# Kernel optimization log

Measured on AMD Instinct MI355X. Metric: run time of the kernel, lower is better.

Reference implementation:

```python
import jax, jax.numpy as jnp
import numpy as np

OS = 14            # output_size
GRID = 2           # ceil(roi_size/OS) = ceil(28/14) = 2 (boxes are built 28x28, sampling_ratio=-1)
NODES = OS * OS    # 196 graph nodes
EPS = 1e-5         # BatchNorm eps
K, B, C, H, W = 256, 4, 256, 112, 112


def _bn_relu(x, g, b, m, v):
    # eval-mode BatchNorm2d followed by ReLU (bn_act_conv prefix)
    s = jax.lax.rsqrt(v + EPS)
    xn = (x - m[None, :, None, None]) * s[None, :, None, None]
    return jax.nn.relu(xn * g[None, :, None, None] + b[None, :, None, None])


def _conv(x, w, b, pad):
    y = jax.lax.conv_general_dilated(x, w, (1, 1), [(pad, pad), (pad, pad)],
                                     dimension_numbers=('NCHW', 'OIHW', 'NCHW'))
    return y + b[None, :, None, None]


def _roi_align(sem, boxes):
    # torchvision roi_align, spatial_scale=1.0, aligned=False, sampling_ratio=-1 (static grid=2)
    Bs, Cc, Hh, Ww = sem.shape
    bidx = boxes[:, 0].astype(jnp.int32)
    x1, y1, x2, y2 = boxes[:, 1], boxes[:, 2], boxes[:, 3], boxes[:, 4]
    bw = jnp.maximum(x2 - x1, 1.0) / OS
    bh = jnp.maximum(y2 - y1, 1.0) / OS
    t = (jnp.arange(OS * GRID, dtype=sem.dtype) + 0.5) / GRID   # pw*GRID+ix collapsed
    xs = x1[:, None] + bw[:, None] * t                          # [K, 28]
    ys = y1[:, None] + bh[:, None] * t

    def prep(c, L):
        m = (c >= -1.0) & (c <= L)
        cc = jnp.clip(c, 0.0, L - 1)
        lo = jnp.floor(cc).astype(jnp.int32)
        hi = jnp.minimum(lo + 1, L - 1)
        return m, lo, hi, cc - lo

    my, yl, yh, ly = prep(ys, Hh)
    mx, xl, xh, lx = prep(xs, Ww)
    semt = jnp.transpose(sem, (0, 2, 3, 1))  # [B,H,W,C]

    def gat(ya, xa):
        return semt[bidx[:, None, None], ya[:, :, None], xa[:, None, :]]  # [K,28,28,C]

    ly_ = ly[:, :, None, None]
    lx_ = lx[:, None, :, None]
    val = (gat(yl, xl) * (1 - ly_) * (1 - lx_) + gat(yl, xh) * (1 - ly_) * lx_
           + gat(yh, xl) * ly_ * (1 - lx_) + gat(yh, xh) * ly_ * lx_)
    val = jnp.where((my[:, :, None] & mx[:, None, :])[..., None], val, 0.0)
    val = val.reshape(-1, OS, GRID, OS, GRID, Cc).mean(axis=(2, 4))  # avg over sampling grid
    return jnp.transpose(val, (0, 3, 1, 2))  # [K,C,14,14]


def _gcn_agg(A, x):
    # PyG gcn_norm on a fully-connected weighted graph (self loops already present):
    # deg[j] = sum_i A[i,j] (scatter on col); out[j] = sum_i d^-1/2[i] A[i,j] d^-1/2[j] x[i]
    deg = A.sum(axis=1)                 # [K,196]
    dis = jax.lax.rsqrt(deg)            # sigmoid weights > 0 => no zero degree
    Nrm = dis[:, :, None] * A * dis[:, None, :]
    return jnp.einsum('kij,kif->kjf', Nrm, x)


def _forward(roi_feature, semantic, boxes,
             bn_sem_g, bn_sem_b, bn_sem_m, bn_sem_v, conv_sem_w, conv_sem_b,
             bn_fpn_g, bn_fpn_b, bn_fpn_m, bn_fpn_v, conv_fpn_w, conv_fpn_b,
             bn_aff_g, bn_aff_b, bn_aff_m, bn_aff_v, conv_aff_w, conv_aff_b,
             gcn1_w, gcn1_b, gcn2_w, gcn2_b):
    roi_sem = _roi_align(semantic, boxes)                                   # [K,256,14,14]
    a = (_conv(_bn_relu(roi_sem, bn_sem_g, bn_sem_b, bn_sem_m, bn_sem_v), conv_sem_w, conv_sem_b, 1)
         + _conv(_bn_relu(roi_feature, bn_fpn_g, bn_fpn_b, bn_fpn_m, bn_fpn_v), conv_fpn_w, conv_fpn_b, 1))
    aff = _conv(_bn_relu(a, bn_aff_g, bn_aff_b, bn_aff_m, bn_aff_v), conv_aff_w, conv_aff_b, 0)
    A = jax.nn.sigmoid(aff.reshape(-1, NODES, NODES))                       # [K,196,196]
    X = roi_feature.reshape(-1, C, NODES).transpose(0, 2, 1)                # [K,196,256] node feats
    x1 = jax.nn.relu(_gcn_agg(A, X @ gcn1_w) + gcn1_b)                      # GCNConv(256,16)+ReLU
    x2 = _gcn_agg(A, x1 @ gcn2_w) + gcn2_b                                  # GCNConv(16,256)
    emb = x2.transpose(0, 2, 1).reshape(-1, C, OS, OS)
    return roi_sem + emb


def setup_inputs() -> dict:
    key = jax.random.key(0)
    ks = jax.random.split(key, 24)
    roi_feature = jax.random.normal(ks[0], (K, C, OS, OS), jnp.float32)
    semantic = jax.random.normal(ks[1], (B, C, H, W), jnp.float32)
    bidx = jax.random.randint(ks[2], (K,), 0, B).astype(jnp.float32)
    xy = jax.random.uniform(ks[3], (K, 2), jnp.float32, 0.0, float(H - 28))
    boxes = jnp.concatenate([bidx[:, None], xy, xy + 28.0], axis=1)  # (idx,x1,y1,x2,y2), 28x28 boxes

    def bn(kg, c):
        k1, k2, k3, k4 = jax.random.split(kg, 4)
        return (jax.random.normal(k1, (c,)) * 0.1 + 1.0,
                jax.random.normal(k2, (c,)) * 0.1,
                jax.random.normal(k3, (c,)) * 0.1,
                jax.random.uniform(k4, (c,), jnp.float32, 0.5, 1.5))
    bn_sem = bn(ks[4], C); bn_fpn = bn(ks[5], C); bn_aff = bn(ks[6], 64)
    inp = {
        'roi_feature': roi_feature, 'semantic': semantic, 'boxes': boxes,
        'bn_sem_g': bn_sem[0], 'bn_sem_b': bn_sem[1], 'bn_sem_m': bn_sem[2], 'bn_sem_v': bn_sem[3],
        'conv_sem_w': jax.random.normal(ks[7], (64, C, 3, 3)) * 0.02,
        'conv_sem_b': jax.random.normal(ks[8], (64,)) * 0.02,
        'bn_fpn_g': bn_fpn[0], 'bn_fpn_b': bn_fpn[1], 'bn_fpn_m': bn_fpn[2], 'bn_fpn_v': bn_fpn[3],
        'conv_fpn_w': jax.random.normal(ks[9], (64, C, 3, 3)) * 0.02,
        'conv_fpn_b': jax.random.normal(ks[10], (64,)) * 0.02,
        'bn_aff_g': bn_aff[0], 'bn_aff_b': bn_aff[1], 'bn_aff_m': bn_aff[2], 'bn_aff_v': bn_aff[3],
        'conv_aff_w': jax.random.normal(ks[11], (NODES, 64, 1, 1)) * 0.05,
        'conv_aff_b': jax.random.normal(ks[12], (NODES,)) * 0.05,
        'gcn1_w': jax.random.normal(ks[13], (C, 16)) * 0.05,
        'gcn1_b': jax.random.normal(ks[14], (16,)) * 0.05,
        'gcn2_w': jax.random.normal(ks[15], (16, C)) * 0.05,
        'gcn2_b': jax.random.normal(ks[16], (C,)) * 0.05,
    }
    return inp


def reference(roi_feature, semantic, boxes,
              bn_sem_g, bn_sem_b, bn_sem_m, bn_sem_v, conv_sem_w, conv_sem_b,
              bn_fpn_g, bn_fpn_b, bn_fpn_m, bn_fpn_v, conv_fpn_w, conv_fpn_b,
              bn_aff_g, bn_aff_b, bn_aff_m, bn_aff_v, conv_aff_w, conv_aff_b,
              gcn1_w, gcn1_b, gcn2_w, gcn2_b):
    return _forward(roi_feature, semantic, boxes,
                    bn_sem_g, bn_sem_b, bn_sem_m, bn_sem_v, conv_sem_w, conv_sem_b,
                    bn_fpn_g, bn_fpn_b, bn_fpn_m, bn_fpn_v, conv_fpn_w, conv_fpn_b,
                    bn_aff_g, bn_aff_b, bn_aff_m, bn_aff_v, conv_aff_w, conv_aff_b,
                    gcn1_w, gcn1_b, gcn2_w, gcn2_b)
```

## Files before the change

### kernel.cpp

```cpp
#include <hip/hip_runtime.h>
#include <hip/hip_bf16.h>

#define KBOX 256
#define CCH  256
#define NODES 196
#define OS 14

typedef __attribute__((ext_vector_type(8))) short  bf16x8;
typedef __attribute__((ext_vector_type(8))) unsigned short u16x8;
typedef __attribute__((ext_vector_type(4))) float  f32x4;
typedef __attribute__((ext_vector_type(4))) short  s16x4;
typedef __attribute__((ext_vector_type(4))) int    i32x4;

__device__ __forceinline__ short f2bf(float x) {
  __hip_bfloat16 h = __float2bfloat16(x);
  return *reinterpret_cast<short*>(&h);
}
__device__ __forceinline__ float bf2f(unsigned short u) {
  unsigned int x = ((unsigned int)u) << 16;
  union { unsigned int i; float f; } c; c.i = x;
  return c.f;
}

#define MFMA16 __builtin_amdgcn_mfma_f32_16x16x32_bf16

__global__ __launch_bounds__(256) void prep_kernel(
    const float* __restrict__ bn_sem_g, const float* __restrict__ bn_sem_b,
    const float* __restrict__ bn_sem_m, const float* __restrict__ bn_sem_v,
    const float* __restrict__ conv_sem_w, const float* __restrict__ conv_sem_b,
    const float* __restrict__ bn_fpn_g, const float* __restrict__ bn_fpn_b,
    const float* __restrict__ bn_fpn_m, const float* __restrict__ bn_fpn_v,
    const float* __restrict__ conv_fpn_w, const float* __restrict__ conv_fpn_b,
    const float* __restrict__ bn_aff_g, const float* __restrict__ bn_aff_b,
    const float* __restrict__ bn_aff_m, const float* __restrict__ bn_aff_v,
    const float* __restrict__ conv_aff_w, const float* __restrict__ g1w,
    const float* __restrict__ g2w,
    float* __restrict__ ss_sem, float* __restrict__ ss_fpn, float* __restrict__ ss_aff2,
    short* __restrict__ wfrag, short* __restrict__ wafrag, short* __restrict__ g1wf,
    short* __restrict__ g2wf)
{
  int gid = blockIdx.x * blockDim.x + threadIdx.x;
  int gsz = gridDim.x * blockDim.x;
  for (int c = gid; c < 256; c += gsz) {
    float s = bn_sem_g[c] * rsqrtf(bn_sem_v[c] + 1e-5f);
    ss_sem[c] = s; ss_sem[256 + c] = bn_sem_b[c] - bn_sem_m[c] * s;
    float s2 = bn_fpn_g[c] * rsqrtf(bn_fpn_v[c] + 1e-5f);
    ss_fpn[c] = s2; ss_fpn[256 + c] = bn_fpn_b[c] - bn_fpn_m[c] * s2;
  }
  for (int c = gid; c < 64; c += gsz) {
    float s = bn_aff_g[c] * rsqrtf(bn_aff_v[c] + 1e-5f);
    float sh = bn_aff_b[c] - bn_aff_m[c] * s;
    float bias = conv_sem_b[c] + conv_fpn_b[c];
    ss_aff2[c] = s; ss_aff2[64 + c] = bias * s + sh;
  }
  for (int idx = gid; idx < 144 * 4 * 64 * 8; idx += gsz) {
    int e = idx & 7, lane = (idx >> 3) & 63, nt = (idx >> 9) & 3, kstep = idx >> 11;
    int src = kstep / 72, rem = kstep % 72, icc = rem / 9, pos = rem % 9;
    int ky = pos / 3, kx = pos % 3;
    int oc = nt * 16 + (lane & 15);
    int ic = icc * 32 + (lane >> 4) * 8 + e;
    const float* w = src ? conv_fpn_w : conv_sem_w;
    wfrag[idx] = f2bf(w[((oc * 256 + ic) * 3 + ky) * 3 + kx]);
  }
  for (int idx = gid; idx < 2 * 13 * 64 * 8; idx += gsz) {
    int t = idx;
    int e = t & 7; t >>= 3;
    int lane = t & 63; t >>= 6;
    int nt = t % 13; int s = t / 13;
    int i = nt * 16 + (lane & 15);
    int ic = s * 32 + (lane >> 4) * 8 + e;
    wafrag[idx] = f2bf(i < NODES ? conv_aff_w[i * 64 + ic] : 0.f);
  }
  for (int idx = gid; idx < 8 * 64 * 8; idx += gsz) {
    int e = idx & 7, lane = (idx >> 3) & 63, ks = idx >> 9;
    int ic = ks * 32 + (lane >> 4) * 8 + e;
    int f = lane & 15;
    g1wf[idx] = f2bf(g1w[ic * 16 + f]);
  }
  for (int idx = gid; idx < 16 * 64 * 8; idx += gsz) {
    int e = idx & 7, lane = (idx >> 3) & 63, ct = idx >> 9;
    int kk = (lane >> 4) * 8 + e;
    int c = ct * 16 + (lane & 15);
    g2wf[idx] = f2bf(kk < 16 ? g2w[kk * 256 + c] : 0.f);
  }
}

__global__ __launch_bounds__(256) void transpose_bf16_kernel(
    const float* __restrict__ in, unsigned short* __restrict__ out, int C, int HW)
{
  __shared__ float tile[64][65];
  int nh = (HW + 63) >> 6;
  int bi = blockIdx.x;
  int cb = bi % (C >> 6); bi /= (C >> 6);
  int hb = bi % nh; int b = bi / nh;
  int tx = threadIdx.x & 63, ty = threadIdx.x >> 6;
  const float* inb = in + (size_t)b * C * HW;
  unsigned short* outb = out + (size_t)b * HW * C;
  #pragma unroll
  for (int i = ty; i < 64; i += 4) {
    int c = cb * 64 + i, hw = hb * 64 + tx;
    tile[i][tx] = (hw < HW) ? inb[(size_t)c * HW + hw] : 0.f;
  }
  __syncthreads();
  int cp = threadIdx.x & 31;
  #pragma unroll
  for (int i = (int)(threadIdx.x >> 5); i < 64; i += 8) {
    int hw = hb * 64 + i;
    if (hw < HW) {
      ushort2 v;
      v.x = (unsigned short)f2bf(tile[cp * 2][i]);
      v.y = (unsigned short)f2bf(tile[cp * 2 + 1][i]);
      *(ushort2*)&outb[(size_t)hw * C + cb * 64 + cp * 2] = v;
    }
  }
}

__global__ __launch_bounds__(512) void roi_align_kernel(
    const unsigned short* __restrict__ semt, const float* __restrict__ boxes,
    unsigned short* __restrict__ roi_sem)
{
  __shared__ unsigned short slab[5][29][256];
  int kb = blockIdx.x / 7, g = blockIdx.x % 7;
  int tid = threadIdx.x, wave = tid >> 6, lane = tid & 63;
  const float* bx = boxes + kb * 5;
  int bb = (int)bx[0];
  float x1 = bx[1], y1 = bx[2];
  float xb = x1 + 0.5f, yv = y1 + 0.5f;
  int X0 = (int)floorf(xb); float fx = xb - (float)X0;
  int Y0 = (int)floorf(yv); float fy = yv - (float)Y0;
  const unsigned short* base = semt + (size_t)bb * 12544 * 256;
  #pragma unroll
  for (int i = 0; i < 19; ++i) {
    int s = wave + i * 8;
    if (s < 145) {
      int r = s / 29, xi = s - r * 29;
      int yr = min(Y0 + 4 * g + r, 111);
      int xc = min(X0 + xi, 111);
      *(s16x4*)&slab[r][xi][lane * 4] =
          *(const s16x4*)(base + ((size_t)yr * 112 + xc) * 256 + lane * 4);
    }
  }
  __syncthreads();
  int c2 = tid & 127, grp = tid >> 7;
  int oyl = grp >> 1, og = grp & 1;
  int rb = oyl * 2;
  float w0 = 1.f - fy;
  unsigned short* op = roi_sem + (((size_t)kb * NODES) + (2 * g + oyl) * OS) * 256 + c2 * 2;
  #pragma unroll
  for (int oxs = 0; oxs < 7; ++oxs) {
    int ox = og * 7 + oxs;
    float o0 = 0.f, o1 = 0.f;
    #pragma unroll
    for (int xi = 0; xi < 3; ++xi) {
      float xw = (xi == 0) ? (1.f - fx) : (xi == 1 ? 1.f : fx);
      const unsigned short* p0 = &slab[rb][2 * ox + xi][c2 * 2];
      const unsigned short* p1 = &slab[rb + 1][2 * ox + xi][c2 * 2];
      const unsigned short* p2 = &slab[rb + 2][2 * ox + xi][c2 * 2];
      o0 += xw * (w0 * bf2f(p0[0]) + bf2f(p1[0]) + fy * bf2f(p2[0]));
      o1 += xw * (w0 * bf2f(p0[1]) + bf2f(p1[1]) + fy * bf2f(p2[1]));
    }
    ushort2 v;
    v.x = (unsigned short)f2bf(o0 * 0.25f);
    v.y = (unsigned short)f2bf(o1 * 0.25f);
    *(ushort2*)(op + (size_t)ox * 256) = v;
  }
}

__global__ __launch_bounds__(512) void conv_ab_kernel(
    const unsigned short* __restrict__ roi_sem, const unsigned short* __restrict__ roif,
    const float* __restrict__ ss_sem, const float* __restrict__ ss_fpn,
    const float* __restrict__ ss_aff2, const short* __restrict__ wfrag,
    short* __restrict__ a_rel)
{
  __shared__ short inLDS[198 * 268];
  __shared__ float scA[64], cmbA[64];
  const int k = blockIdx.x;
  const int tid = threadIdx.x;
  const int wave = tid >> 6, lane = tid & 63;
  const int l15 = lane & 15, lq = lane >> 4;
  const int pg = wave >> 1, ng = wave & 1;
  const int p0 = (pg == 0) ? 0 : (pg * 2 + 1);
  const int p1 = p0 + ((pg == 0) ? 3 : 2);

  if (tid < 64) { scA[tid] = ss_aff2[tid]; cmbA[tid] = ss_aff2[64 + tid]; }
  if (tid < 34) {
    bf16x8 z = {};
    *(bf16x8*)&inLDS[196 * 268 + tid * 8] = z;
  }

  int oyA[13], oxA[13];
  #pragma unroll
  for (int mt = 0; mt < 13; ++mt) {
    int j = mt * 16 + l15;
    int oy = j / 14;
    oyA[mt] = oy; oxA[mt] = j - oy * 14;
  }
  const int c0 = (tid & 31) * 8;

  f32x4 acc[13][2];
  #pragma unroll
  for (int mt = 0; mt < 13; ++mt) {
    acc[mt][0] = f32x4{0.f, 0.f, 0.f, 0.f};
    acc[mt][1] = f32x4{0.f, 0.f, 0.f, 0.f};
  }

  for (int src = 0; src < 2; ++src) {
    const unsigned short* inp = (src ? roif : roi_sem) + (size_t)k * NODES * CCH;
    const float* ss = src ? ss_fpn : ss_sem;
    f32x4 sc0 = *(const f32x4*)(ss + c0);
    f32x4 sc1 = *(const f32x4*)(ss + c0 + 4);
    f32x4 sh0 = *(const f32x4*)(ss + 256 + c0);
    f32x4 sh1 = *(const f32x4*)(ss + 256 + c0 + 4);
    __syncthreads();
    #pragma unroll
    for (int i = 0; i < 12; ++i) {
      int j = (tid >> 5) + i * 16;
      u16x8 v = *(const u16x8*)(inp + (size_t)j * 256 + c0);
      bf16x8 pk;
      #pragma unroll
      for (int u = 0; u < 4; ++u) pk[u] = f2bf(fmaxf(bf2f(v[u]) * sc0[u] + sh0[u], 0.f));
      #pragma unroll
      for (int u = 0; u < 4; ++u) pk[4 + u] = f2bf(fmaxf(bf2f(v[4 + u]) * sc1[u] + sh1[u], 0.f));
      *(bf16x8*)&inLDS[j * 268 + c0] = pk;
    }
    if (tid < 128) {
      int j = 192 + (tid >> 5);
      u16x8 v = *(const u16x8*)(inp + (size_t)j * 256 + c0);
      bf16x8 pk;
      #pragma unroll
      for (int u = 0; u < 4; ++u) pk[u] = f2bf(fmaxf(bf2f(v[u]) * sc0[u] + sh0[u], 0.f));
      #pragma unroll
      for (int u = 0; u < 4; ++u) pk[4 + u] = f2bf(fmaxf(bf2f(v[4 + u]) * sc1[u] + sh1[u], 0.f));
      *(bf16x8*)&inLDS[j * 268 + c0] = pk;
    }
    __syncthreads();

    for (int pos = p0; pos < p1; ++pos) {
      int ky = pos / 3 - 1, kx = pos % 3 - 1;
      int np[13];
      #pragma unroll
      for (int mt = 0; mt < 13; ++mt) {
        int ny = oyA[mt] + ky, nx = oxA[mt] + kx;
        bool v = ((unsigned)ny < 14u) & ((unsigned)nx < 14u) & ((mt * 16 + l15) < 196);
        np[mt] = v ? (ny * 14 + nx) : 196;
      }
      #pragma unroll
      for (int icc = 0; icc < 8; ++icc) {
        const short* wp = wfrag +
            ((size_t)((src * 72 + icc * 9 + pos) * 4 + ng * 2) * 64 + lane) * 8;
        bf16x8 b0 = *(const bf16x8*)wp;
        bf16x8 b1 = *(const bf16x8*)(wp + 512);
        #pragma unroll
        for (int mt = 0; mt < 13; ++mt) {
          bf16x8 a = *(const bf16x8*)&inLDS[np[mt] * 268 + icc * 32 + lq * 8];
          acc[mt][0] = MFMA16(a, b0, acc[mt][0], 0, 0, 0);
          acc[mt][1] = MFMA16(a, b1, acc[mt][1], 0, 0, 0);
        }
      }
    }
  }

  float* red = (float*)inLDS;
  __syncthreads();
  if (pg == 1 || pg == 3) {
    float* dst = red + (size_t)((pg >> 1) * 2 + ng) * 6272;
    #pragma unroll
    for (int mt = 0; mt < 13; ++mt)
      #pragma unroll
      for (int nn = 0; nn < 2; ++nn)
        #pragma unroll
        for (int r = 0; r < 4; ++r) {
          int j = mt * 16 + lq * 4 + r;
          if (j < 196) dst[j * 32 + nn * 16 + l15] = acc[mt][nn][r];
        }
  }
  __syncthreads();
  if (pg == 0 || pg == 2) {
    const float* sb = red + (size_t)((pg >> 1) * 2 + ng) * 6272;
    #pragma unroll
    for (int mt = 0; mt < 13; ++mt)
      #pragma unroll
      for (int nn = 0; nn < 2; ++nn)
        #pragma unroll
        for (int r = 0; r < 4; ++r) {
          int j = mt * 16 + lq * 4 + r;
          if (j < 196) acc[mt][nn][r] += sb[j * 32 + nn * 16 + l15];
        }
  }
  __syncthreads();
  if (pg == 2) {
    float* dst = red + (size_t)ng * 6272;
    #pragma unroll
    for (int mt = 0; mt < 13; ++mt)
      #pragma unroll
      for (int nn = 0; nn < 2; ++nn)
        #pragma unroll
        for (int r = 0; r < 4; ++r) {
          int j = mt * 16 + lq * 4 + r;
          if (j < 196) dst[j * 32 + nn * 16 + l15] = acc[mt][nn][r];
        }
  }
  __syncthreads();
  if (pg == 0) {
    const float* sb = red + (size_t)ng * 6272;
    short* op = a_rel + (size_t)k * 12544;
    #pragma unroll
    for (int mt = 0; mt < 13; ++mt)
      #pragma unroll
      for (int nn = 0; nn < 2; ++nn) {
        int oc = (ng * 2 + nn) * 16 + l15;
        float sa = scA[oc], cb = cmbA[oc];
        #pragma unroll
        for (int r = 0; r < 4; ++r) {
          int j = mt * 16 + lq * 4 + r;
          if (j < 196) {
            float t = acc[mt][nn][r] + sb[j * 32 + nn * 16 + l15];
            op[j * 64 + oc] = f2bf(fmaxf(t * sa + cb, 0.f));
          }
        }
      }
  }
}

__global__ __launch_bounds__(1024, 1) void graph_kernel(
    const short* __restrict__ a_rel, const short* __restrict__ wafrag,
    const float* __restrict__ aff_b, const short* __restrict__ g1wf,
    const float* __restrict__ g1b, const unsigned short* __restrict__ roif_bf,
    const short* __restrict__ g2wf, const float* __restrict__ g2b,
    const unsigned short* __restrict__ roi_sem, float* __restrict__ outp)
{
  __shared__ __align__(16) char smem[125840];
  const int tid = threadIdx.x, wave = tid >> 6, lane = tid & 63;
  const int l15 = lane & 15, lq = lane >> 4;
  const int k = blockIdx.x;

  char*  Ab   = smem;
  short* wa   = (short*)(smem + 96512);
  short* yfr  = (short*)(smem + 96512);
  short* zsf  = (short*)(smem + 103680);
  float* dsl  = (float*)(smem + 123136);
  float* g1bl = (float*)(smem + 123968);
  float* g2bl = (float*)(smem + 124032);
  float* affb = (float*)(smem + 125056);

  const bool wv13 = (wave < 13);
  const int jr  = wave * 16 + l15;
  const int jrc = min(jr, 195);
  const i32x4 z4 = {};

  bf16x8 af0 = {}, af1 = {};
  if (wv13) {
    const short* ap = a_rel + (size_t)k * 12544 + jrc * 64 + lq * 8;
    af0 = *(const bf16x8*)ap;
    af1 = *(const bf16x8*)(ap + 32);
  }
  {
    i32x4 w0 = ((const i32x4*)wafrag)[tid];
    i32x4 w1 = z4;
    if (tid < 640) w1 = ((const i32x4*)wafrag)[1024 + tid];
    if (tid < 832) {
      int r = tid >> 2, q = tid & 3;
      *(i32x4*)(Ab + r * 464 + 384 + q * 16) = z4;
    }
    if (tid < 196) affb[tid] = aff_b[tid];
    if (tid < 256) g2bl[tid] = g2b[tid];
    if (tid < 16)  g1bl[tid] = g1b[tid];
    ((i32x4*)wa)[tid] = w0;
    if (tid < 640) ((i32x4*)wa)[1024 + tid] = w1;
  }
  __syncthreads();

  if (wv13) {
    float rsum[4] = {0.f, 0.f, 0.f, 0.f};
    #pragma unroll
    for (int n = 0; n < 13; ++n) {
      bf16x8 b0 = *(const bf16x8*)(wa + (n * 64 + lane) * 8);
      bf16x8 b1 = *(const bf16x8*)(wa + ((13 + n) * 64 + lane) * 8);
      f32x4 acc = {0.f, 0.f, 0.f, 0.f};
      acc = MFMA16(af0, b0, acc, 0, 0, 0);
      acc = MFMA16(af1, b1, acc, 0, 0, 0);
      int i = n * 16 + l15;
      bool iv = (i < 196);
      float bv = affb[iv ? i : 0];
      #pragma unroll
      for (int r = 0; r < 4; ++r) {
        float v = acc[r] + bv;
        float s = 1.f / (1.f + __expf(-v));
        if (iv) {
          rsum[r] += s;
          *(short*)(Ab + (wave * 16 + lq * 4 + r) * 464 + i * 2) = f2bf(s);
        }
      }
    }
    #pragma unroll
    for (int r = 0; r < 4; ++r) {
      float v = rsum[r];
      v += __shfl_xor(v, 1); v += __shfl_xor(v, 2);
      v += __shfl_xor(v, 4); v += __shfl_xor(v, 8);
      int j = wave * 16 + lq * 4 + r;
      if (l15 == 0 && j < 196) dsl[j] = rsqrtf(v);
    }
  }
  __syncthreads();

  *(i32x4*)(smem + 96512 + tid * 16) = z4;
  if (tid < 256) *(i32x4*)(smem + 96512 + (1024 + tid) * 16) = z4;
  f32x4 xacc = {0.f, 0.f, 0.f, 0.f};
  if (wv13) {
    const unsigned short* Xp = roif_bf + (size_t)k * 50176 + (size_t)jrc * 256 + lq * 8;
    #pragma unroll
    for (int ks = 0; ks < 8; ++ks) {
      bf16x8 xa = *(const bf16x8*)(Xp + ks * 32);
      bf16x8 xb = *(const bf16x8*)(g1wf + (ks * 64 + lane) * 8);
      xacc = MFMA16(xa, xb, xacc, 0, 0, 0);
    }
  }
  __syncthreads();

  if (wv13) {
    #pragma unroll
    for (int r = 0; r < 4; ++r) {
      int i = wave * 16 + lq * 4 + r;
      if (i < 196) {
        float yv = dsl[i] * xacc[r];
        yfr[((i >> 5) * 64 + ((i >> 3) & 3) * 16 + l15) * 8 + (i & 7)] = f2bf(yv);
      }
    }
  }
  __syncthreads();

  f32x4 g0 = {0.f, 0.f, 0.f, 0.f};
  if (wv13) {
    #pragma unroll
    for (int ks = 0; ks < 7; ++ks) {
      bf16x8 bb = *(const bf16x8*)(yfr + (ks * 64 + lane) * 8);
      bf16x8 a0 = *(const bf16x8*)(Ab + jr * 464 + ks * 64 + lq * 16);
      g0 = MFMA16(a0, bb, g0, 0, 0, 0);
    }
  }
  __syncthreads();
  if (wv13) {
    #pragma unroll
    for (int r = 0; r < 4; ++r) {
      int i = wave * 16 + lq * 4 + r;
      if (i < 196) {
        float d = dsl[i];
        float x1v = fmaxf(g0[r] * d + g1bl[l15], 0.f);
        yfr[((i >> 5) * 64 + ((i >> 3) & 3) * 16 + l15) * 8 + (i & 7)] = f2bf(d * x1v);
      }
    }
  }
  __syncthreads();

  if (wv13) {
    f32x4 z0 = {0.f, 0.f, 0.f, 0.f};
    #pragma unroll
    for (int ks = 0; ks < 7; ++ks) {
      bf16x8 bb = *(const bf16x8*)(yfr + (ks * 64 + lane) * 8);
      bf16x8 a0 = *(const bf16x8*)(Ab + jr * 464 + ks * 64 + lq * 16);
      z0 = MFMA16(a0, bb, z0, 0, 0, 0);
    }
    #pragma unroll
    for (int r = 0; r < 4; ++r) {
      int j = wave * 16 + lq * 4 + r;
      if (j < 196) {
        float zv = z0[r] * dsl[j];
        zsf[((j >> 4) * 64 + (l15 >> 3) * 16 + (j & 15)) * 8 + (l15 & 7)] = f2bf(zv);
      }
    }
  }
  __syncthreads();

  {
    bf16x8 wf = *(const bf16x8*)(g2wf + (wave * 64 + lane) * 8);
    const unsigned short* rsmk = roi_sem + (size_t)k * 50176;
    float* op = outp + (size_t)k * 50176;
    float gbv[4];
    #pragma unroll
    for (int r = 0; r < 4; ++r) gbv[r] = g2bl[wave * 16 + lq * 4 + r];
    #pragma unroll
    for (int jt = 0; jt < 13; ++jt) {
      bf16x8 zb = *(const bf16x8*)(zsf + (jt * 64 + lane) * 8);
      f32x4 d = {0.f, 0.f, 0.f, 0.f};
      d = MFMA16(wf, zb, d, 0, 0, 0);
      int j = jt * 16 + l15;
      if (j < 196) {
        #pragma unroll
        for (int r = 0; r < 4; ++r) {
          int c = wave * 16 + lq * 4 + r;
          op[(size_t)c * 196 + j] = d[r] + gbv[r] + bf2f(rsmk[(size_t)j * 256 + c]);
        }
      }
    }
  }
}

extern "C" void kernel_launch(void* const* d_in, const int* in_sizes, int n_in,
                              void* d_out, int out_size, void* d_ws, size_t ws_size,
                              hipStream_t stream) {
  const float* roi_feature = (const float*)d_in[0];
  const float* semantic    = (const float*)d_in[1];
  const float* boxes       = (const float*)d_in[2];
  const float* bn_sem_g = (const float*)d_in[3];
  const float* bn_sem_b = (const float*)d_in[4];
  const float* bn_sem_m = (const float*)d_in[5];
  const float* bn_sem_v = (const float*)d_in[6];
  const float* conv_sem_w = (const float*)d_in[7];
  const float* conv_sem_b = (const float*)d_in[8];
  const float* bn_fpn_g = (const float*)d_in[9];
  const float* bn_fpn_b = (const float*)d_in[10];
  const float* bn_fpn_m = (const float*)d_in[11];
  const float* bn_fpn_v = (const float*)d_in[12];
  const float* conv_fpn_w = (const float*)d_in[13];
  const float* conv_fpn_b = (const float*)d_in[14];
  const float* bn_aff_g = (const float*)d_in[15];
  const float* bn_aff_b = (const float*)d_in[16];
  const float* bn_aff_m = (const float*)d_in[17];
  const float* bn_aff_v = (const float*)d_in[18];
  const float* conv_aff_w = (const float*)d_in[19];
  const float* conv_aff_b = (const float*)d_in[20];
  const float* gcn1_w = (const float*)d_in[21];
  const float* gcn1_b = (const float*)d_in[22];
  const float* gcn2_w = (const float*)d_in[23];
  const float* gcn2_b = (const float*)d_in[24];

  const size_t FT = (size_t)KBOX * NODES * CCH;
  unsigned short* ws16      = (unsigned short*)d_ws;
  unsigned short* semt_bf   = ws16;
  unsigned short* roif_bf   = semt_bf + FT;
  unsigned short* roi_sem_b = roif_bf + FT;
  short*          a_rel     = (short*)(roi_sem_b + FT);
  float*          ss_sem    = (float*)(a_rel + 3211264);
  float*          ss_fpn    = ss_sem + 512;
  float*          ss_aff2   = ss_fpn + 512;
  short*          wfrag     = (short*)(ss_aff2 + 128);
  short*          wafrag    = wfrag + 294912;
  short*          g1wf      = wafrag + 13312;
  short*          g2wf      = g1wf + 4096;

  prep_kernel<<<256, 256, 0, stream>>>(
      bn_sem_g, bn_sem_b, bn_sem_m, bn_sem_v, conv_sem_w, conv_sem_b,
      bn_fpn_g, bn_fpn_b, bn_fpn_m, bn_fpn_v, conv_fpn_w, conv_fpn_b,
      bn_aff_g, bn_aff_b, bn_aff_m, bn_aff_v, conv_aff_w, gcn1_w, gcn2_w,
      ss_sem, ss_fpn, ss_aff2, wfrag, wafrag, g1wf, g2wf);

  transpose_bf16_kernel<<<4 * 196 * 4, 256, 0, stream>>>(semantic, semt_bf, 256, 12544);
  transpose_bf16_kernel<<<4 * 4 * 256, 256, 0, stream>>>(roi_feature, roif_bf, 256, 196);
  roi_align_kernel<<<KBOX * 7, 512, 0, stream>>>(semt_bf, boxes, roi_sem_b);
  conv_ab_kernel<<<KBOX, 512, 0, stream>>>(roi_sem_b, roif_bf, ss_sem, ss_fpn, ss_aff2,
                                           wfrag, a_rel);
  graph_kernel<<<KBOX, 1024, 0, stream>>>(a_rel, wafrag, conv_aff_b, g1wf, gcn1_b, roif_bf,
                                          g2wf, gcn2_b, roi_sem_b, (float*)d_out);
}
```

Baseline: 163.4 us.

## Repartition conv_ab over spatial rows with 32x32 MFMA, dropping cross-wave reduction

The 3x3 conv in conv_ab_kernel switches from 16x16x32 MFMAs, where waves split the kernel positions, to 32x32x16 MFMAs. Each of seven waves now owns 32 output pixels and all 64 output channels, so every wave covers all 9 positions and 8 channel chunks. That removes the multi-stage LDS reduction between waves and its barriers, and cuts accumulator registers. The weight fragment layout in prep_kernel is rebuilt for the 32-lane MFMA B operand, and the LDS row pitch changes from 268 to 264. In exchange, each wave must load all weights from global memory, and the new LDS pitch may cause more bank conflicts.

```diff
diff --git a/kernel.cpp b/kernel.cpp
--- a/kernel.cpp
+++ b/kernel.cpp
@@ -9,6 +9,7 @@
 typedef __attribute__((ext_vector_type(8))) short  bf16x8;
 typedef __attribute__((ext_vector_type(8))) unsigned short u16x8;
 typedef __attribute__((ext_vector_type(4))) float  f32x4;
+typedef __attribute__((ext_vector_type(16))) float f32x16;
 typedef __attribute__((ext_vector_type(4))) short  s16x4;
 typedef __attribute__((ext_vector_type(4))) int    i32x4;
 
@@ -23,6 +24,7 @@
 }
 
 #define MFMA16 __builtin_amdgcn_mfma_f32_16x16x32_bf16
+#define MFMA32 __builtin_amdgcn_mfma_f32_32x32x16_bf16
 
 __global__ __launch_bounds__(256) void prep_kernel(
     const float* __restrict__ bn_sem_g, const float* __restrict__ bn_sem_b,
@@ -53,12 +55,15 @@
     float bias = conv_sem_b[c] + conv_fpn_b[c];
     ss_aff2[c] = s; ss_aff2[64 + c] = bias * s + sh;
   }
-  for (int idx = gid; idx < 144 * 4 * 64 * 8; idx += gsz) {
-    int e = idx & 7, lane = (idx >> 3) & 63, nt = (idx >> 9) & 3, kstep = idx >> 11;
-    int src = kstep / 72, rem = kstep % 72, icc = rem / 9, pos = rem % 9;
+  for (int idx = gid; idx < 2 * 8 * 9 * 2 * 2 * 512; idx += gsz) {
+    int e = idx & 7, lane = (idx >> 3) & 63;
+    int nt = (idx >> 9) & 1, ksub = (idx >> 10) & 1;
+    int pk = idx >> 11;
+    int pos = pk % 9, t2 = pk / 9;
+    int icc = t2 & 7, src = t2 >> 3;
     int ky = pos / 3, kx = pos % 3;
-    int oc = nt * 16 + (lane & 15);
-    int ic = icc * 32 + (lane >> 4) * 8 + e;
+    int oc = nt * 32 + (lane & 31);
+    int ic = icc * 32 + ksub * 16 + (lane >> 5) * 8 + e;
     const float* w = src ? conv_fpn_w : conv_sem_w;
     wfrag[idx] = f2bf(w[((oc * 256 + ic) * 3 + ky) * 3 + kx]);
   }
@@ -166,43 +171,33 @@
   }
 }
 
-__global__ __launch_bounds__(512) void conv_ab_kernel(
+__global__ __launch_bounds__(448) void conv_ab_kernel(
     const unsigned short* __restrict__ roi_sem, const unsigned short* __restrict__ roif,
     const float* __restrict__ ss_sem, const float* __restrict__ ss_fpn,
     const float* __restrict__ ss_aff2, const short* __restrict__ wfrag,
     short* __restrict__ a_rel)
 {
-  __shared__ short inLDS[198 * 268];
+  __shared__ short inLDS[197 * 264 + 8];
   __shared__ float scA[64], cmbA[64];
   const int k = blockIdx.x;
   const int tid = threadIdx.x;
   const int wave = tid >> 6, lane = tid & 63;
-  const int l15 = lane & 15, lq = lane >> 4;
-  const int pg = wave >> 1, ng = wave & 1;
-  const int p0 = (pg == 0) ? 0 : (pg * 2 + 1);
-  const int p1 = p0 + ((pg == 0) ? 3 : 2);
+  const int l31 = lane & 31, lg = lane >> 5;
+  const int j = wave * 32 + l31;
+  const int oy = j / 14, ox = j - oy * 14;
+  const bool jv = (j < 196);
 
   if (tid < 64) { scA[tid] = ss_aff2[tid]; cmbA[tid] = ss_aff2[64 + tid]; }
-  if (tid < 34) {
-    bf16x8 z = {};
-    *(bf16x8*)&inLDS[196 * 268 + tid * 8] = z;
-  }
-
-  int oyA[13], oxA[13];
-  #pragma unroll
-  for (int mt = 0; mt < 13; ++mt) {
-    int j = mt * 16 + l15;
-    int oy = j / 14;
-    oyA[mt] = oy; oxA[mt] = j - oy * 14;
-  }
+  if (tid < 32) { bf16x8 z = {}; *(bf16x8*)&inLDS[196 * 264 + tid * 8] = z; }
+
+  f32x16 acc[2];
+  #pragma unroll
+  for (int nt = 0; nt < 2; ++nt)
+    #pragma unroll
+    for (int i = 0; i < 16; ++i) acc[nt][i] = 0.f;
+
   const int c0 = (tid & 31) * 8;
-
-  f32x4 acc[13][2];
-  #pragma unroll
-  for (int mt = 0; mt < 13; ++mt) {
-    acc[mt][0] = f32x4{0.f, 0.f, 0.f, 0.f};
-    acc[mt][1] = f32x4{0.f, 0.f, 0.f, 0.f};
-  }
+  const int rgrp = tid >> 5;
 
   for (int src = 0; src < 2; ++src) {
     const unsigned short* inp = (src ? roif : roi_sem) + (size_t)k * NODES * CCH;
@@ -213,112 +208,52 @@
     f32x4 sh1 = *(const f32x4*)(ss + 256 + c0 + 4);
     __syncthreads();
     #pragma unroll
-    for (int i = 0; i < 12; ++i) {
-      int j = (tid >> 5) + i * 16;
-      u16x8 v = *(const u16x8*)(inp + (size_t)j * 256 + c0);
+    for (int i = 0; i < 14; ++i) {
+      int r = rgrp + i * 14;
+      u16x8 v = *(const u16x8*)(inp + (size_t)r * 256 + c0);
       bf16x8 pk;
       #pragma unroll
       for (int u = 0; u < 4; ++u) pk[u] = f2bf(fmaxf(bf2f(v[u]) * sc0[u] + sh0[u], 0.f));
       #pragma unroll
       for (int u = 0; u < 4; ++u) pk[4 + u] = f2bf(fmaxf(bf2f(v[4 + u]) * sc1[u] + sh1[u], 0.f));
-      *(bf16x8*)&inLDS[j * 268 + c0] = pk;
-    }
-    if (tid < 128) {
-      int j = 192 + (tid >> 5);
-      u16x8 v = *(const u16x8*)(inp + (size_t)j * 256 + c0);
-      bf16x8 pk;
+      *(bf16x8*)&inLDS[r * 264 + c0] = pk;
+    }
+    __syncthreads();
+
+    const short* wsrc = wfrag + (size_t)src * 147456;
+    for (int icc = 0; icc < 8; ++icc) {
+      const short* wicc = wsrc + (size_t)icc * 18432;
       #pragma unroll
-      for (int u = 0; u < 4; ++u) pk[u] = f2bf(fmaxf(bf2f(v[u]) * sc0[u] + sh0[u], 0.f));
-      #pragma unroll
-      for (int u = 0; u < 4; ++u) pk[4 + u] = f2bf(fmaxf(bf2f(v[4 + u]) * sc1[u] + sh1[u], 0.f));
-      *(bf16x8*)&inLDS[j * 268 + c0] = pk;
-    }
-    __syncthreads();
-
-    for (int pos = p0; pos < p1; ++pos) {
-      int ky = pos / 3 - 1, kx = pos % 3 - 1;
-      int np[13];
-      #pragma unroll
-      for (int mt = 0; mt < 13; ++mt) {
-        int ny = oyA[mt] + ky, nx = oxA[mt] + kx;
-        bool v = ((unsigned)ny < 14u) & ((unsigned)nx < 14u) & ((mt * 16 + l15) < 196);
-        np[mt] = v ? (ny * 14 + nx) : 196;
-      }
-      #pragma unroll
-      for (int icc = 0; icc < 8; ++icc) {
-        const short* wp = wfrag +
-            ((size_t)((src * 72 + icc * 9 + pos) * 4 + ng * 2) * 64 + lane) * 8;
-        bf16x8 b0 = *(const bf16x8*)wp;
-        bf16x8 b1 = *(const bf16x8*)(wp + 512);
+      for (int pos = 0; pos < 9; ++pos) {
+        int ky = pos / 3 - 1, kx = pos % 3 - 1;
+        int ny = oy + ky, nx = ox + kx;
+        bool v = jv & ((unsigned)ny < 14u) & ((unsigned)nx < 14u);
+        int np = v ? (ny * 14 + nx) : 196;
+        const short* ap = &inLDS[np * 264 + icc * 32 + lg * 8];
         #pragma unroll
-        for (int mt = 0; mt < 13; ++mt) {
-          bf16x8 a = *(const bf16x8*)&inLDS[np[mt] * 268 + icc * 32 + lq * 8];
-          acc[mt][0] = MFMA16(a, b0, acc[mt][0], 0, 0, 0);
-          acc[mt][1] = MFMA16(a, b1, acc[mt][1], 0, 0, 0);
+        for (int ksub = 0; ksub < 2; ++ksub) {
+          bf16x8 a = *(const bf16x8*)(ap + ksub * 16);
+          const short* wp = wicc + (pos * 2 + ksub) * 1024 + lane * 8;
+          bf16x8 b0 = *(const bf16x8*)wp;
+          bf16x8 b1 = *(const bf16x8*)(wp + 512);
+          acc[0] = MFMA32(a, b0, acc[0], 0, 0, 0);
+          acc[1] = MFMA32(a, b1, acc[1], 0, 0, 0);
         }
       }
     }
   }
 
-  float* red = (float*)inLDS;
-  __syncthreads();
-  if (pg == 1 || pg == 3) {
-    float* dst = red + (size_t)((pg >> 1) * 2 + ng) * 6272;
-    #pragma unroll
-    for (int mt = 0; mt < 13; ++mt)
-      #pragma unroll
-      for (int nn = 0; nn < 2; ++nn)
-        #pragma unroll
-        for (int r = 0; r < 4; ++r) {
-          int j = mt * 16 + lq * 4 + r;
-          if (j < 196) dst[j * 32 + nn * 16 + l15] = acc[mt][nn][r];
-        }
-  }
-  __syncthreads();
-  if (pg == 0 || pg == 2) {
-    const float* sb = red + (size_t)((pg >> 1) * 2 + ng) * 6272;
-    #pragma unroll
-    for (int mt = 0; mt < 13; ++mt)
-      #pragma unroll
-      for (int nn = 0; nn < 2; ++nn)
-        #pragma unroll
-        for (int r = 0; r < 4; ++r) {
-          int j = mt * 16 + lq * 4 + r;
-          if (j < 196) acc[mt][nn][r] += sb[j * 32 + nn * 16 + l15];
-        }
-  }
-  __syncthreads();
-  if (pg == 2) {
-    float* dst = red + (size_t)ng * 6272;
-    #pragma unroll
-    for (int mt = 0; mt < 13; ++mt)
-      #pragma unroll
-      for (int nn = 0; nn < 2; ++nn)
-        #pragma unroll
-        for (int r = 0; r < 4; ++r) {
-          int j = mt * 16 + lq * 4 + r;
-          if (j < 196) dst[j * 32 + nn * 16 + l15] = acc[mt][nn][r];
-        }
-  }
-  __syncthreads();
-  if (pg == 0) {
-    const float* sb = red + (size_t)ng * 6272;
-    short* op = a_rel + (size_t)k * 12544;
-    #pragma unroll
-    for (int mt = 0; mt < 13; ++mt)
-      #pragma unroll
-      for (int nn = 0; nn < 2; ++nn) {
-        int oc = (ng * 2 + nn) * 16 + l15;
-        float sa = scA[oc], cb = cmbA[oc];
-        #pragma unroll
-        for (int r = 0; r < 4; ++r) {
-          int j = mt * 16 + lq * 4 + r;
-          if (j < 196) {
-            float t = acc[mt][nn][r] + sb[j * 32 + nn * 16 + l15];
-            op[j * 64 + oc] = f2bf(fmaxf(t * sa + cb, 0.f));
-          }
-        }
-      }
+  short* op = a_rel + (size_t)k * 12544;
+  #pragma unroll
+  for (int nt = 0; nt < 2; ++nt) {
+    int oc = nt * 32 + l31;
+    float sa = scA[oc], cb = cmbA[oc];
+    #pragma unroll
+    for (int r = 0; r < 16; ++r) {
+      int row = wave * 32 + (r & 3) + 8 * (r >> 2) + 4 * lg;
+      if (row < 196)
+        op[row * 64 + oc] = f2bf(fmaxf(acc[nt][r] * sa + cb, 0.f));
+    }
   }
 }
 
@@ -547,7 +482,7 @@
   transpose_bf16_kernel<<<4 * 196 * 4, 256, 0, stream>>>(semantic, semt_bf, 256, 12544);
   transpose_bf16_kernel<<<4 * 4 * 256, 256, 0, stream>>>(roi_feature, roif_bf, 256, 196);
   roi_align_kernel<<<KBOX * 7, 512, 0, stream>>>(semt_bf, boxes, roi_sem_b);
-  conv_ab_kernel<<<KBOX, 512, 0, stream>>>(roi_sem_b, roif_bf, ss_sem, ss_fpn, ss_aff2,
+  conv_ab_kernel<<<KBOX, 448, 0, stream>>>(roi_sem_b, roif_bf, ss_sem, ss_fpn, ss_aff2,
                                            wfrag, a_rel);
   graph_kernel<<<KBOX, 1024, 0, stream>>>(a_rel, wafrag, conv_aff_b, g1wf, gcn1_b, roif_bf,
                                           g2wf, gcn2_b, roi_sem_b, (float*)d_out);
```

Result: slower. 190.2 us (+16.4%).
